# Optimization experiments

Hardware: AMD Instinct MI355X
Metric: run time of the kernel (lower is better)

Reference implementation:

```python
import jax, jax.numpy as jnp
import numpy as np

# PointPillars PillarFeatureNet defaults
VX, VY, VZ = 0.2, 0.2, 4.0
X_OFF = VX / 2 + 0.0
Y_OFF = VY / 2 + (-40.0)
Z_OFF = VZ / 2 + (-3.0)
BN_EPS = 1e-3
N, M, C_RAW, C_IN, C_OUT = 100000, 32, 4, 10, 64


def setup_inputs() -> dict:
    key = jax.random.key(0)
    k1, k2, k3, k4, k5, k6 = jax.random.split(key, 6)
    features = jax.random.normal(k1, (N, M, C_RAW), dtype=jnp.float32)
    num_points = jax.random.randint(k2, (N,), 1, M + 1, dtype=jnp.int32)
    coors = jax.random.randint(k3, (N, 4), 0, 400, dtype=jnp.int32)
    # PFNLayer params: Linear(10 -> 64, bias=False) + BatchNorm1d(64) (eval stats)
    W = jax.random.normal(k4, (C_OUT, C_IN), dtype=jnp.float32) * (1.0 / np.sqrt(C_IN))
    gamma = jnp.ones((C_OUT,), jnp.float32)
    beta = jnp.zeros((C_OUT,), jnp.float32)
    running_mean = jax.random.normal(k5, (C_OUT,), dtype=jnp.float32) * 0.1
    running_var = jnp.abs(jax.random.normal(k6, (C_OUT,), dtype=jnp.float32)) * 0.1 + 0.9
    return {"features": features, "num_points": num_points, "coors": coors,
            "W": W, "gamma": gamma, "beta": beta,
            "running_mean": running_mean, "running_var": running_var}


def reference(features, num_points, coors, W, gamma, beta, running_mean, running_var):
    np_f = num_points.astype(features.dtype)[:, None, None]            # (N,1,1)
    xyz = features[:, :, :3]                                           # (N,M,3)
    # cluster center offset
    points_mean = jnp.sum(xyz, axis=1, keepdims=True) / np_f           # (N,1,3)
    f_cluster = xyz - points_mean                                      # (N,M,3)
    # voxel center offset (coors layout: [batch, z, y, x])
    cz = coors[:, 0].astype(features.dtype)[:, None]
    cy = coors[:, 1].astype(features.dtype)[:, None]
    cx = coors[:, 2].astype(features.dtype)[:, None]
    f_center = jnp.stack([
        features[:, :, 0] - (cx * VX + X_OFF),
        features[:, :, 1] - (cy * VY + Y_OFF),
        features[:, :, 2] - (cz * VZ + Z_OFF),
    ], axis=-1)                                                        # (N,M,3)
    feats = jnp.concatenate([features, f_cluster, f_center], axis=-1)  # (N,M,10)
    # padding mask
    mask = (jnp.arange(M, dtype=jnp.int32)[None, :] < num_points[:, None])
    feats = feats * mask[:, :, None].astype(feats.dtype)
    # PFNLayer: Linear -> BN(eval) -> GELU -> max over points
    x = jnp.einsum('nmc,oc->nmo', feats, W)                            # (N,M,64)
    inv_std = jax.lax.rsqrt(running_var + BN_EPS)
    x = (x - running_mean) * (inv_std * gamma) + beta
    x = jax.nn.gelu(x, approximate=False)
    return jnp.max(x, axis=1)                                          # (N,64)
```

## Files before the change

### kernel.cpp

```cpp
#include <hip/hip_runtime.h>
#include <cmath>


typedef float f32x2 __attribute__((ext_vector_type(2)));

__device__ __forceinline__ float max3f(float a, float b, float c) {
    float d;
    asm("v_max3_f32 %0, %1, %2, %3" : "=v"(d) : "v"(a), "v"(b), "v"(c));
    return d;
}
__device__ __forceinline__ float min3f(float a, float b, float c) {
    float d;
    asm("v_min3_f32 %0, %1, %2, %3" : "=v"(d) : "v"(a), "v"(b), "v"(c));
    return d;
}
__device__ __forceinline__ f32x2 pk_fma(f32x2 a, f32x2 b, f32x2 c) {
    f32x2 d;
    asm("v_pk_fma_f32 %0, %1, %2, %3" : "=v"(d) : "v"(a), "v"(b), "v"(c));
    return d;
}
__device__ __forceinline__ f32x2 pk_mul(f32x2 a, f32x2 b) {
    f32x2 d;
    asm("v_pk_mul_f32 %0, %1, %2" : "=v"(d) : "v"(a), "v"(b));
    return d;
}
__device__ __forceinline__ float fast_exp2(float a) {
    float d;
    asm("v_exp_f32 %0, %1" : "=v"(d) : "v"(a));
    return d;
}

__device__ __forceinline__ f32x2 gelu2(f32x2 x) {
    const f32x2 c_t    = {0.70710678f, 0.70710678f};
    const f32x2 c_p    = {0.3275911f, 0.3275911f};
    const f32x2 c_one  = {1.0f, 1.0f};
    const f32x2 c_half = {0.5f, 0.5f};
    const f32x2 b1 = {-0.254829592f, -0.254829592f};
    const f32x2 b2 = { 0.284496736f,  0.284496736f};
    const f32x2 b3 = {-1.421413741f, -1.421413741f};
    const f32x2 b4 = { 1.453152027f,  1.453152027f};
    const f32x2 b5 = {-1.061405429f, -1.061405429f};
    const f32x2 c_k = {-1.02013963f, -1.02013963f};

    f32x2 ax = {fabsf(x.x), fabsf(x.y)};
    f32x2 t  = pk_mul(ax, c_t);
    f32x2 u  = pk_fma(t, c_p, c_one);
    f32x2 s  = {__builtin_amdgcn_rcpf(u.x), __builtin_amdgcn_rcpf(u.y)};
    f32x2 poly = pk_fma(b5, s, b4);
    poly = pk_fma(poly, s, b3);
    poly = pk_fma(poly, s, b2);
    poly = pk_fma(poly, s, b1);
    poly = pk_mul(poly, s);
    f32x2 t3  = pk_mul(ax, c_k);
    f32x2 arg = pk_mul(t, t3);
    f32x2 e   = {fast_exp2(arg.x), fast_exp2(arg.y)};
    f32x2 E   = pk_fma(poly, e, c_one);
    f32x2 h   = pk_mul(x, c_half);
    f32x2 hax = pk_mul(ax, c_half);
    return pk_fma(hax, E, h);
}

__global__ __launch_bounds__(256) void pfn_kernel(
    const float* __restrict__ features,
    const int*   __restrict__ num_points,
    const int*   __restrict__ coors,
    const float* __restrict__ W,
    const float* __restrict__ gamma,
    const float* __restrict__ beta,
    const float* __restrict__ rmean,
    const float* __restrict__ rvar,
    float*       __restrict__ out,
    int nTotal)
{
    __shared__ float4 lds[4][64];

    const int lane = threadIdx.x & 63;
    const int wid  = threadIdx.x >> 6;
    const int waveGlobal = blockIdx.x * 4 + wid;
    const int waveCount  = gridDim.x * 4;
    const int nPairs = (nTotal + 1) >> 1;

    const int o = lane;
    const float w0 = W[o*10+0], w1 = W[o*10+1], w2 = W[o*10+2], w3 = W[o*10+3],
                w4 = W[o*10+4], w5 = W[o*10+5], w6 = W[o*10+6], w7 = W[o*10+7],
                w8 = W[o*10+8], w9 = W[o*10+9];
    const float a = gamma[o] / sqrtf(rvar[o] + 1e-3f);
    const float b = fmaf(-rmean[o], a, beta[o]);
    const float A0 = a*(w0+w4+w7), A1 = a*(w1+w5+w8), A2 = a*(w2+w6+w9), A3 = a*w3;

    for (int p = waveGlobal; p < nPairs; p += waveCount) {
        const int iA = 2*p;
        const bool hasB = (2*p + 1 < nTotal);
        const int iB = hasB ? (2*p + 1) : (nTotal - 1);

        const float4* fb = reinterpret_cast<const float4*>(features) + (size_t)p * 64;
        float4 f = fb[lane];
        lds[wid][lane] = f;

        float sx = f.x, sy = f.y, sz = f.z;
        #pragma unroll
        for (int d = 1; d < 32; d <<= 1) {
            sx += __shfl_xor(sx, d);
            sy += __shfl_xor(sy, d);
            sz += __shfl_xor(sz, d);
        }
        const float tx = __shfl_xor(sx, 32), ty = __shfl_xor(sy, 32), tz = __shfl_xor(sz, 32);
        const bool lo = (lane < 32);
        const float sAx = lo ? sx : tx, sAy = lo ? sy : ty, sAz = lo ? sz : tz;
        const float sBx = lo ? tx : sx, sBy = lo ? ty : sy, sBz = lo ? tz : sz;

        const int nA = num_points[iA];
        const int nB = num_points[iB];
        const int4 cA = reinterpret_cast<const int4*>(coors)[iA];
        const int4 cB = reinterpret_cast<const int4*>(coors)[iB];

        const float rcA = __builtin_amdgcn_rcpf((float)nA);
        const float rcB = __builtin_amdgcn_rcpf((float)nB);
        const float mAx = sAx * rcA, mAy = sAy * rcA, mAz = sAz * rcA;
        const float mBx = sBx * rcB, mBy = sBy * rcB, mBz = sBz * rcB;

        const float ccxA = fmaf((float)cA.z, 0.2f,   0.1f);
        const float ccyA = fmaf((float)cA.y, 0.2f, -39.9f);
        const float cczA = fmaf((float)cA.x, 4.0f,  -1.0f);
        const float ccxB = fmaf((float)cB.z, 0.2f,   0.1f);
        const float ccyB = fmaf((float)cB.y, 0.2f, -39.9f);
        const float cczB = fmaf((float)cB.x, 4.0f,  -1.0f);

        const float KA = -(mAx*w4 + mAy*w5 + mAz*w6 + ccxA*w7 + ccyA*w8 + cczA*w9);
        const float KB = -(mBx*w4 + mBy*w5 + mBz*w6 + ccxB*w7 + ccyB*w8 + cczB*w9);
        const float CA = fmaf(a, KA, b);
        const float CB = fmaf(a, KB, b);

        __asm__ volatile("s_waitcnt lgkmcnt(0)" ::: "memory");

        float vmaxA = -INFINITY, vminA = INFINITY;
        {
            const float4* la = &lds[wid][0];
            int m = 0;
            for (; m + 2 <= nA; m += 2) {
                float4 t0 = la[m];
                float4 t1 = la[m+1];
                float y0 = fmaf(t0.x, A0, fmaf(t0.y, A1, fmaf(t0.z, A2, fmaf(t0.w, A3, CA))));
                float y1 = fmaf(t1.x, A0, fmaf(t1.y, A1, fmaf(t1.z, A2, fmaf(t1.w, A3, CA))));
                vmaxA = max3f(vmaxA, y0, y1);
                vminA = min3f(vminA, y0, y1);
            }
            if (m < nA) {
                float4 t = la[m];
                float y = fmaf(t.x, A0, fmaf(t.y, A1, fmaf(t.z, A2, fmaf(t.w, A3, CA))));
                vmaxA = fmaxf(vmaxA, y);
                vminA = fminf(vminA, y);
            }
        }
        float vmaxB = -INFINITY, vminB = INFINITY;
        {
            const float4* lb = &lds[wid][32];
            int m = 0;
            for (; m + 2 <= nB; m += 2) {
                float4 t0 = lb[m];
                float4 t1 = lb[m+1];
                float y0 = fmaf(t0.x, A0, fmaf(t0.y, A1, fmaf(t0.z, A2, fmaf(t0.w, A3, CB))));
                float y1 = fmaf(t1.x, A0, fmaf(t1.y, A1, fmaf(t1.z, A2, fmaf(t1.w, A3, CB))));
                vmaxB = max3f(vmaxB, y0, y1);
                vminB = min3f(vminB, y0, y1);
            }
            if (m < nB) {
                float4 t = lb[m];
                float y = fmaf(t.x, A0, fmaf(t.y, A1, fmaf(t.z, A2, fmaf(t.w, A3, CB))));
                vmaxB = fmaxf(vmaxB, y);
                vminB = fminf(vminB, y);
            }
        }
        if (nA < 32) { vmaxA = fmaxf(vmaxA, b); vminA = fminf(vminA, b); }
        if (nB < 32) { vmaxB = fmaxf(vmaxB, b); vminB = fminf(vminB, b); }

        const f32x2 gA = gelu2((f32x2){vmaxA, vminA});
        const f32x2 gB = gelu2((f32x2){vmaxB, vminB});
        const float rAo = fmaxf(gA.x, gA.y);
        const float rBo = fmaxf(gB.x, gB.y);

        out[(size_t)iA * 64 + o] = rAo;
        if (hasB) out[(size_t)iB * 64 + o] = rBo;
    }
}

extern "C" void kernel_launch(void* const* d_in, const int* in_sizes, int n_in,
                              void* d_out, int out_size, void* d_ws, size_t ws_size,
                              hipStream_t stream) {
    const float* features   = (const float*)d_in[0];
    const int*   num_points = (const int*)  d_in[1];
    const int*   coors      = (const int*)  d_in[2];
    const float* W          = (const float*)d_in[3];
    const float* gamma      = (const float*)d_in[4];
    const float* beta       = (const float*)d_in[5];
    const float* rmean      = (const float*)d_in[6];
    const float* rvar       = (const float*)d_in[7];
    float* out = (float*)d_out;

    const int nTotal = in_sizes[1];

    const int nPairs = (nTotal + 1) / 2;
    int blocks = (nPairs + 7) / 8;
    if (blocks < 1) blocks = 1;
    pfn_kernel<<<blocks, 256, 0, stream>>>(features, num_points, coors, W,
                                           gamma, beta, rmean, rvar, out, nTotal);
}
```

Baseline: 123.5 us.

## Process two pillar pairs per wave with DPP reductions and prefetched LDS scans

Replaces the grid-stride loop with a fixed assignment of two pillar pairs per wave. Both pairs' feature, count and coordinate loads are issued up front so they overlap. Half-wave sums now use DPP row ops plus readlane instead of xor shuffles. The per-pillar constant is added after the min/max scan rather than inside every FMA chain, and the scan loop software-prefetches the next two LDS entries. The launch still uses (nPairs+7)/8 blocks of four waves, so every pair gets covered. The explicit lgkmcnt wait was replaced by a compiler barrier, and the scan may read up to two entries past a segment.

After: 122.1 us, median of 2. Within noise of the previous version (-1.1%).

```diff
diff --git a/kernel.cpp b/kernel.cpp
--- a/kernel.cpp
+++ b/kernel.cpp
@@ -34,7 +34,6 @@
     const f32x2 c_t    = {0.70710678f, 0.70710678f};
     const f32x2 c_p    = {0.3275911f, 0.3275911f};
     const f32x2 c_one  = {1.0f, 1.0f};
-    const f32x2 c_half = {0.5f, 0.5f};
     const f32x2 b1 = {-0.254829592f, -0.254829592f};
     const f32x2 b2 = { 0.284496736f,  0.284496736f};
     const f32x2 b3 = {-1.421413741f, -1.421413741f};
@@ -55,9 +54,46 @@
     f32x2 arg = pk_mul(t, t3);
     f32x2 e   = {fast_exp2(arg.x), fast_exp2(arg.y)};
     f32x2 E   = pk_fma(poly, e, c_one);
-    f32x2 h   = pk_mul(x, c_half);
-    f32x2 hax = pk_mul(ax, c_half);
+    f32x2 h   = pk_mul(x, (f32x2){0.5f, 0.5f});
+    f32x2 hax = pk_mul(ax, (f32x2){0.5f, 0.5f});
     return pk_fma(hax, E, h);
+}
+
+template <int CTRL, int ROW_MASK>
+__device__ __forceinline__ float dpp_add(float v) {
+    int x = __builtin_amdgcn_update_dpp(0, __builtin_bit_cast(int, v), CTRL, ROW_MASK, 0xf, false);
+    return v + __builtin_bit_cast(float, x);
+}
+__device__ __forceinline__ void half_sums(float v, float& sA, float& sB) {
+    v = dpp_add<0x111, 0xf>(v);
+    v = dpp_add<0x112, 0xf>(v);
+    v = dpp_add<0x114, 0xf>(v);
+    v = dpp_add<0x118, 0xf>(v);
+    v = dpp_add<0x142, 0xa>(v);
+    sA = __builtin_bit_cast(float, __builtin_amdgcn_readlane(__builtin_bit_cast(int, v), 31));
+    sB = __builtin_bit_cast(float, __builtin_amdgcn_readlane(__builtin_bit_cast(int, v), 63));
+}
+
+__device__ __forceinline__ void scan_minmax(const float4* base, int n,
+                                            float A0, float A1, float A2, float A3,
+                                            float& dmax, float& dmin) {
+    float vmax = -INFINITY, vmin = INFINITY;
+    float4 t0 = base[0], t1 = base[1];
+    int m = 0;
+    for (; m + 2 <= n; m += 2) {
+        float4 u0 = base[m + 2], u1 = base[m + 3];
+        float y0 = fmaf(t0.x, A0, fmaf(t0.y, A1, fmaf(t0.z, A2, t0.w * A3)));
+        float y1 = fmaf(t1.x, A0, fmaf(t1.y, A1, fmaf(t1.z, A2, t1.w * A3)));
+        vmax = max3f(vmax, y0, y1);
+        vmin = min3f(vmin, y0, y1);
+        t0 = u0; t1 = u1;
+    }
+    if (m < n) {
+        float y = fmaf(t0.x, A0, fmaf(t0.y, A1, fmaf(t0.z, A2, t0.w * A3)));
+        vmax = fmaxf(vmax, y);
+        vmin = fminf(vmin, y);
+    }
+    dmax = vmax; dmin = vmin;
 }
 
 __global__ __launch_bounds__(256) void pfn_kernel(
@@ -72,13 +108,33 @@
     float*       __restrict__ out,
     int nTotal)
 {
-    __shared__ float4 lds[4][64];
+    __shared__ float4 lds[520];
 
     const int lane = threadIdx.x & 63;
     const int wid  = threadIdx.x >> 6;
-    const int waveGlobal = blockIdx.x * 4 + wid;
-    const int waveCount  = gridDim.x * 4;
+    const int wv   = blockIdx.x * 4 + wid;
     const int nPairs = (nTotal + 1) >> 1;
+    const int p0 = wv * 2;
+    if (p0 >= nPairs) return;
+    const int p1 = (p0 + 1 < nPairs) ? (p0 + 1) : p0;
+
+    const float4* fbase = reinterpret_cast<const float4*>(features);
+    const float4 f0 = fbase[(size_t)p0 * 64 + lane];
+    const float4 f1 = fbase[(size_t)p1 * 64 + lane];
+
+    const int i0A = 2 * p0;
+    const bool h0B = (2 * p0 + 1 < nTotal);
+    const int i0B = h0B ? (2 * p0 + 1) : (nTotal - 1);
+    const int i1A = 2 * p1;
+    const bool h1B = (2 * p1 + 1 < nTotal);
+    const int i1B = h1B ? (2 * p1 + 1) : (nTotal - 1);
+
+    const int n0A = num_points[i0A], n0B = num_points[i0B];
+    const int n1A = num_points[i1A], n1B = num_points[i1B];
+    const int4 c0A = reinterpret_cast<const int4*>(coors)[i0A];
+    const int4 c0B = reinterpret_cast<const int4*>(coors)[i0B];
+    const int4 c1A = reinterpret_cast<const int4*>(coors)[i1A];
+    const int4 c1B = reinterpret_cast<const int4*>(coors)[i1B];
 
     const int o = lane;
     const float w0 = W[o*10+0], w1 = W[o*10+1], w2 = W[o*10+2], w3 = W[o*10+3],
@@ -88,100 +144,70 @@
     const float b = fmaf(-rmean[o], a, beta[o]);
     const float A0 = a*(w0+w4+w7), A1 = a*(w1+w5+w8), A2 = a*(w2+w6+w9), A3 = a*w3;
 
-    for (int p = waveGlobal; p < nPairs; p += waveCount) {
-        const int iA = 2*p;
-        const bool hasB = (2*p + 1 < nTotal);
-        const int iB = hasB ? (2*p + 1) : (nTotal - 1);
-
-        const float4* fb = reinterpret_cast<const float4*>(features) + (size_t)p * 64;
-        float4 f = fb[lane];
-        lds[wid][lane] = f;
-
-        float sx = f.x, sy = f.y, sz = f.z;
-        #pragma unroll
-        for (int d = 1; d < 32; d <<= 1) {
-            sx += __shfl_xor(sx, d);
-            sy += __shfl_xor(sy, d);
-            sz += __shfl_xor(sz, d);
-        }
-        const float tx = __shfl_xor(sx, 32), ty = __shfl_xor(sy, 32), tz = __shfl_xor(sz, 32);
-        const bool lo = (lane < 32);
-        const float sAx = lo ? sx : tx, sAy = lo ? sy : ty, sAz = lo ? sz : tz;
-        const float sBx = lo ? tx : sx, sBy = lo ? ty : sy, sBz = lo ? tz : sz;
-
-        const int nA = num_points[iA];
-        const int nB = num_points[iB];
-        const int4 cA = reinterpret_cast<const int4*>(coors)[iA];
-        const int4 cB = reinterpret_cast<const int4*>(coors)[iB];
-
-        const float rcA = __builtin_amdgcn_rcpf((float)nA);
-        const float rcB = __builtin_amdgcn_rcpf((float)nB);
-        const float mAx = sAx * rcA, mAy = sAy * rcA, mAz = sAz * rcA;
-        const float mBx = sBx * rcB, mBy = sBy * rcB, mBz = sBz * rcB;
-
-        const float ccxA = fmaf((float)cA.z, 0.2f,   0.1f);
-        const float ccyA = fmaf((float)cA.y, 0.2f, -39.9f);
-        const float cczA = fmaf((float)cA.x, 4.0f,  -1.0f);
-        const float ccxB = fmaf((float)cB.z, 0.2f,   0.1f);
-        const float ccyB = fmaf((float)cB.y, 0.2f, -39.9f);
-        const float cczB = fmaf((float)cB.x, 4.0f,  -1.0f);
-
-        const float KA = -(mAx*w4 + mAy*w5 + mAz*w6 + ccxA*w7 + ccyA*w8 + cczA*w9);
-        const float KB = -(mBx*w4 + mBy*w5 + mBz*w6 + ccxB*w7 + ccyB*w8 + cczB*w9);
-        const float CA = fmaf(a, KA, b);
-        const float CB = fmaf(a, KB, b);
-
-        __asm__ volatile("s_waitcnt lgkmcnt(0)" ::: "memory");
-
-        float vmaxA = -INFINITY, vminA = INFINITY;
-        {
-            const float4* la = &lds[wid][0];
-            int m = 0;
-            for (; m + 2 <= nA; m += 2) {
-                float4 t0 = la[m];
-                float4 t1 = la[m+1];
-                float y0 = fmaf(t0.x, A0, fmaf(t0.y, A1, fmaf(t0.z, A2, fmaf(t0.w, A3, CA))));
-                float y1 = fmaf(t1.x, A0, fmaf(t1.y, A1, fmaf(t1.z, A2, fmaf(t1.w, A3, CA))));
-                vmaxA = max3f(vmaxA, y0, y1);
-                vminA = min3f(vminA, y0, y1);
-            }
-            if (m < nA) {
-                float4 t = la[m];
-                float y = fmaf(t.x, A0, fmaf(t.y, A1, fmaf(t.z, A2, fmaf(t.w, A3, CA))));
-                vmaxA = fmaxf(vmaxA, y);
-                vminA = fminf(vminA, y);
-            }
-        }
-        float vmaxB = -INFINITY, vminB = INFINITY;
-        {
-            const float4* lb = &lds[wid][32];
-            int m = 0;
-            for (; m + 2 <= nB; m += 2) {
-                float4 t0 = lb[m];
-                float4 t1 = lb[m+1];
-                float y0 = fmaf(t0.x, A0, fmaf(t0.y, A1, fmaf(t0.z, A2, fmaf(t0.w, A3, CB))));
-                float y1 = fmaf(t1.x, A0, fmaf(t1.y, A1, fmaf(t1.z, A2, fmaf(t1.w, A3, CB))));
-                vmaxB = max3f(vmaxB, y0, y1);
-                vminB = min3f(vminB, y0, y1);
-            }
-            if (m < nB) {
-                float4 t = lb[m];
-                float y = fmaf(t.x, A0, fmaf(t.y, A1, fmaf(t.z, A2, fmaf(t.w, A3, CB))));
-                vmaxB = fmaxf(vmaxB, y);
-                vminB = fminf(vminB, y);
-            }
-        }
-        if (nA < 32) { vmaxA = fmaxf(vmaxA, b); vminA = fminf(vminA, b); }
-        if (nB < 32) { vmaxB = fmaxf(vmaxB, b); vminB = fminf(vminB, b); }
-
-        const f32x2 gA = gelu2((f32x2){vmaxA, vminA});
-        const f32x2 gB = gelu2((f32x2){vmaxB, vminB});
-        const float rAo = fmaxf(gA.x, gA.y);
-        const float rBo = fmaxf(gB.x, gB.y);
-
-        out[(size_t)iA * 64 + o] = rAo;
-        if (hasB) out[(size_t)iB * 64 + o] = rBo;
-    }
+    float4* slot = &lds[wid * 128];
+    slot[lane]      = f0;
+    slot[64 + lane] = f1;
+
+    float s0Ax, s0Bx, s0Ay, s0By, s0Az, s0Bz;
+    float s1Ax, s1Bx, s1Ay, s1By, s1Az, s1Bz;
+    half_sums(f0.x, s0Ax, s0Bx);
+    half_sums(f0.y, s0Ay, s0By);
+    half_sums(f0.z, s0Az, s0Bz);
+    half_sums(f1.x, s1Ax, s1Bx);
+    half_sums(f1.y, s1Ay, s1By);
+    half_sums(f1.z, s1Az, s1Bz);
+
+    const float rc0A = __builtin_amdgcn_rcpf((float)n0A);
+    const float rc0B = __builtin_amdgcn_rcpf((float)n0B);
+    const float rc1A = __builtin_amdgcn_rcpf((float)n1A);
+    const float rc1B = __builtin_amdgcn_rcpf((float)n1B);
+
+    const float K0A = -((s0Ax*rc0A)*w4 + (s0Ay*rc0A)*w5 + (s0Az*rc0A)*w6
+                      + fmaf((float)c0A.z, 0.2f, 0.1f)*w7
+                      + fmaf((float)c0A.y, 0.2f, -39.9f)*w8
+                      + fmaf((float)c0A.x, 4.0f, -1.0f)*w9);
+    const float K0B = -((s0Bx*rc0B)*w4 + (s0By*rc0B)*w5 + (s0Bz*rc0B)*w6
+                      + fmaf((float)c0B.z, 0.2f, 0.1f)*w7
+                      + fmaf((float)c0B.y, 0.2f, -39.9f)*w8
+                      + fmaf((float)c0B.x, 4.0f, -1.0f)*w9);
+    const float K1A = -((s1Ax*rc1A)*w4 + (s1Ay*rc1A)*w5 + (s1Az*rc1A)*w6
+                      + fmaf((float)c1A.z, 0.2f, 0.1f)*w7
+                      + fmaf((float)c1A.y, 0.2f, -39.9f)*w8
+                      + fmaf((float)c1A.x, 4.0f, -1.0f)*w9);
+    const float K1B = -((s1Bx*rc1B)*w4 + (s1By*rc1B)*w5 + (s1Bz*rc1B)*w6
+                      + fmaf((float)c1B.z, 0.2f, 0.1f)*w7
+                      + fmaf((float)c1B.y, 0.2f, -39.9f)*w8
+                      + fmaf((float)c1B.x, 4.0f, -1.0f)*w9);
+    const float C0A = fmaf(a, K0A, b), C0B = fmaf(a, K0B, b);
+    const float C1A = fmaf(a, K1A, b), C1B = fmaf(a, K1B, b);
+
+    asm volatile("" ::: "memory");
+
+    float d0Amax, d0Amin, d0Bmax, d0Bmin, d1Amax, d1Amin, d1Bmax, d1Bmin;
+    scan_minmax(slot,      n0A, A0, A1, A2, A3, d0Amax, d0Amin);
+    scan_minmax(slot + 32, n0B, A0, A1, A2, A3, d0Bmax, d0Bmin);
+    scan_minmax(slot + 64, n1A, A0, A1, A2, A3, d1Amax, d1Amin);
+    scan_minmax(slot + 96, n1B, A0, A1, A2, A3, d1Bmax, d1Bmin);
+
+    float vmax0A = d0Amax + C0A, vmin0A = d0Amin + C0A;
+    float vmax0B = d0Bmax + C0B, vmin0B = d0Bmin + C0B;
+    float vmax1A = d1Amax + C1A, vmin1A = d1Amin + C1A;
+    float vmax1B = d1Bmax + C1B, vmin1B = d1Bmin + C1B;
+
+    if (n0A < 32) { vmax0A = fmaxf(vmax0A, b); vmin0A = fminf(vmin0A, b); }
+    if (n0B < 32) { vmax0B = fmaxf(vmax0B, b); vmin0B = fminf(vmin0B, b); }
+    if (n1A < 32) { vmax1A = fmaxf(vmax1A, b); vmin1A = fminf(vmin1A, b); }
+    if (n1B < 32) { vmax1B = fmaxf(vmax1B, b); vmin1B = fminf(vmin1B, b); }
+
+    const f32x2 g0A = gelu2((f32x2){vmax0A, vmin0A});
+    const f32x2 g0B = gelu2((f32x2){vmax0B, vmin0B});
+    const f32x2 g1A = gelu2((f32x2){vmax1A, vmin1A});
+    const f32x2 g1B = gelu2((f32x2){vmax1B, vmin1B});
+
+    out[(size_t)i0A * 64 + o] = fmaxf(g0A.x, g0A.y);
+    if (h0B) out[(size_t)i0B * 64 + o] = fmaxf(g0B.x, g0B.y);
+    out[(size_t)i1A * 64 + o] = fmaxf(g1A.x, g1A.y);
+    if (h1B) out[(size_t)i1B * 64 + o] = fmaxf(g1B.x, g1B.y);
 }
 
 extern "C" void kernel_launch(void* const* d_in, const int* in_sizes, int n_in,
```
